# Optimization experiments

Measured on AMD Instinct MI355X. Metric: run time of the kernel, lower is better.

The kernel has to match this reference:

```python
import jax, jax.numpy as jnp
import numpy as np

B = 8388608  # batch of ODE states
Z_DIM = 4    # [q0, q1, qd0, qd1]


def _potential_sum(q, k1, k2):
    # V = 0.5*k1*q0^2 + 0.5*k2*(q0 - q1)^2, summed over the batch (matches _potential_E)
    return jnp.sum(0.5 * k1[0] * q[:, 0] ** 2 + 0.5 * k2[0] * (q[:, 0] - q[:, 1]) ** 2)


def setup_inputs() -> dict:
    key = jax.random.key(0)
    kx, = jax.random.split(key, 1)
    return {
        "t": jnp.zeros((1,), dtype=jnp.float32),
        "x": jax.random.normal(kx, (B, Z_DIM), dtype=jnp.float32),
        "k1": jnp.ones((1,), dtype=jnp.float32),
        "k2": jnp.ones((1,), dtype=jnp.float32),
    }


def reference(t, x, k1, k2):
    n = x.shape[1] // 2
    q = x[:, :n]    # positions  [B, n]
    qd = x[:, n:]   # velocities [B, n]

    # T = 0.5 * sum(qd^2)  =>  DL_qd = dT/dqd = qd
    # Hessian of DL_qd wrt (q, qd) is [0_{n x n} | I_{n x n}],
    # so DDL_qqd = 0 and DDL_qdqd = I; inv(I) = I.
    # DL_q = d(-V)/dq
    DL_q = -jax.grad(_potential_sum, argnums=0)(q, k1, k2)  # [B, n]

    eye = jnp.eye(n, dtype=x.dtype)  # DDL_qdqd^{-1} (same for every batch element)
    # qdd = einsum('ijk, ij -> ik', DDL_qdqd_inverse, DL_q) with DDL_qdqd_inverse = I
    qdd = jnp.einsum('jk,ij->ik', eye, DL_q)  # [B, n]

    return jnp.concatenate([qd, qdd], axis=1)  # [B, 2n]
```

## Files before the change

kernel.cpp:

```cpp
#include <hip/hip_runtime.h>


typedef float f32x4 __attribute__((ext_vector_type(4)));

#define BLOCK 256
#define RPT   16
#define BATCH 4

__device__ __forceinline__ f32x4 ode(const f32x4 t, const float k1, const float k2) {
    const float d = t.x - t.y;
    f32x4 o;
    o.x = t.z;
    o.y = t.w;
    o.z = -(k1 * t.x + k2 * d);
    o.w = k2 * d;
    return o;
}

__global__ __launch_bounds__(BLOCK) void lagrangian_ode_kernel(
    const f32x4* __restrict__ x,
    const float* __restrict__ k1p,
    const float* __restrict__ k2p,
    f32x4* __restrict__ out,
    int n_rows) {
    const float k1 = k1p[0];
    const float k2 = k2p[0];
    const int chunk = BLOCK * RPT;
    const int base  = blockIdx.x * chunk + threadIdx.x;

    if (base + (RPT - 1) * BLOCK < n_rows) {
        f32x4 v[BATCH], w[BATCH];
#pragma unroll
        for (int r = 0; r < BATCH; ++r) v[r] = x[base + r * BLOCK];

#pragma unroll
        for (int k = 1; k < RPT / BATCH; ++k) {
#pragma unroll
            for (int r = 0; r < BATCH; ++r)
                w[r] = x[base + (k * BATCH + r) * BLOCK];
#pragma unroll
            for (int r = 0; r < BATCH; ++r)
                __builtin_nontemporal_store(ode(v[r], k1, k2),
                                            &out[base + ((k - 1) * BATCH + r) * BLOCK]);
#pragma unroll
            for (int r = 0; r < BATCH; ++r) v[r] = w[r];
        }
#pragma unroll
        for (int r = 0; r < BATCH; ++r)
            __builtin_nontemporal_store(ode(v[r], k1, k2),
                                        &out[base + (RPT - BATCH + r) * BLOCK]);
    } else {
#pragma unroll
        for (int j = 0; j < RPT; ++j) {
            const int i = base + j * BLOCK;
            if (i < n_rows) {
                __builtin_nontemporal_store(ode(x[i], k1, k2), &out[i]);
            }
        }
    }
}

extern "C" void kernel_launch(void* const* d_in, const int* in_sizes, int n_in,
                              void* d_out, int out_size, void* d_ws, size_t ws_size,
                              hipStream_t stream) {
    const f32x4* x  = (const f32x4*)d_in[1];
    const float* k1 = (const float*)d_in[2];
    const float* k2 = (const float*)d_in[3];
    f32x4* out = (f32x4*)d_out;

    int n_rows = in_sizes[1] / 4;
    int rows_per_block = BLOCK * RPT;
    int grid = (n_rows + rows_per_block - 1) / rows_per_block;
    lagrangian_ode_kernel<<<grid, BLOCK, 0, stream>>>(x, k1, k2, out, n_rows);
}
```

Baseline: 242.3 us.

## Switch to fixed 1024-block grid-stride layout with nontemporal loads

Replaces the per-block contiguous chunking with a fixed grid of 1024 blocks where each thread strides across the whole array by the total thread count, handling 32 rows in batches of 8. Loads become nontemporal and the batch width doubles to keep more memory requests in flight. This reduces block launch and scheduling overhead and changes the access interleaving across the device. It depends on n_rows being exactly 32 times the thread count for the fast path; otherwise a serial grid-stride fallback runs, and the fixed grid may leave CUs underused for other sizes.

```diff
diff --git a/kernel.cpp b/kernel.cpp
--- a/kernel.cpp
+++ b/kernel.cpp
@@ -4,8 +4,8 @@
 typedef float f32x4 __attribute__((ext_vector_type(4)));
 
 #define BLOCK 256
-#define RPT   16
-#define BATCH 4
+#define GRID  1024
+#define BATCH 8
 
 __device__ __forceinline__ f32x4 ode(const f32x4 t, const float k1, const float k2) {
     const float d = t.x - t.y;
@@ -25,37 +25,37 @@
     int n_rows) {
     const float k1 = k1p[0];
     const float k2 = k2p[0];
-    const int chunk = BLOCK * RPT;
-    const int base  = blockIdx.x * chunk + threadIdx.x;
+    const int T   = GRID * BLOCK;
+    const int tid = blockIdx.x * BLOCK + threadIdx.x;
 
-    if (base + (RPT - 1) * BLOCK < n_rows) {
-        f32x4 v[BATCH], w[BATCH];
+    int i = tid;
+    f32x4 v[BATCH], w[BATCH];
+
+    if (i + 31 * T < n_rows) {
 #pragma unroll
-        for (int r = 0; r < BATCH; ++r) v[r] = x[base + r * BLOCK];
+        for (int r = 0; r < BATCH; ++r)
+            v[r] = __builtin_nontemporal_load(&x[i + r * T]);
 
 #pragma unroll
-        for (int k = 1; k < RPT / BATCH; ++k) {
+        for (int k = 1; k < 32 / BATCH; ++k) {
 #pragma unroll
             for (int r = 0; r < BATCH; ++r)
-                w[r] = x[base + (k * BATCH + r) * BLOCK];
+                w[r] = __builtin_nontemporal_load(&x[i + (k * BATCH + r) * T]);
 #pragma unroll
             for (int r = 0; r < BATCH; ++r)
                 __builtin_nontemporal_store(ode(v[r], k1, k2),
-                                            &out[base + ((k - 1) * BATCH + r) * BLOCK]);
+                                            &out[i + ((k - 1) * BATCH + r) * T]);
 #pragma unroll
             for (int r = 0; r < BATCH; ++r) v[r] = w[r];
         }
 #pragma unroll
         for (int r = 0; r < BATCH; ++r)
             __builtin_nontemporal_store(ode(v[r], k1, k2),
-                                        &out[base + (RPT - BATCH + r) * BLOCK]);
+                                        &out[i + (32 - BATCH + r) * T]);
     } else {
-#pragma unroll
-        for (int j = 0; j < RPT; ++j) {
-            const int i = base + j * BLOCK;
-            if (i < n_rows) {
-                __builtin_nontemporal_store(ode(x[i], k1, k2), &out[i]);
-            }
+        for (; i < n_rows; i += T) {
+            __builtin_nontemporal_store(ode(__builtin_nontemporal_load(&x[i]), k1, k2),
+                                        &out[i]);
         }
     }
 }
@@ -69,7 +69,5 @@
     f32x4* out = (f32x4*)d_out;
 
     int n_rows = in_sizes[1] / 4;
-    int rows_per_block = BLOCK * RPT;
-    int grid = (n_rows + rows_per_block - 1) / rows_per_block;
-    lagrangian_ode_kernel<<<grid, BLOCK, 0, stream>>>(x, k1, k2, out, n_rows);
+    lagrangian_ode_kernel<<<GRID, BLOCK, 0, stream>>>(x, k1, k2, out, n_rows);
 }
```

Result: no change. 238.1 us (-1.7%).
